# Performance work log

Hardware: AMD Instinct MI355X
Metric: run time of the kernel (lower is better)

Reference implementation:

```python
import jax, jax.numpy as jnp
import numpy as np

N, E, D, L, R = 100000, 500000, 128, 2, 10
EPS = 1e-5  # BatchNorm1d default eps


def setup_inputs() -> dict:
    key = jax.random.key(0)
    ks = jax.random.split(key, 10)
    return {
        "in_node_emb": jax.random.normal(ks[0], (N, D), jnp.float32),
        "in_rel_emb": jax.random.normal(ks[1], (R, D), jnp.float32),
        "w_in": jax.random.normal(ks[2], (L, D, D), jnp.float32) * 0.05,
        "w_out": jax.random.normal(ks[3], (L, D, D), jnp.float32) * 0.05,
        "w_loop": jax.random.normal(ks[4], (L, D, D), jnp.float32) * 0.05,
        "w_rel": jax.random.normal(ks[5], (L, D, D), jnp.float32) * 0.05,
        "loop_rel": jax.random.normal(ks[6], (L, 1, D), jnp.float32) * 0.05,
        "bias": jnp.zeros((L, D), jnp.float32),
        "edge_src": jax.random.randint(ks[7], (E,), 0, N),
        "edge_dst": jax.random.randint(ks[8], (E,), 0, N),
        "edge_type": jax.random.randint(ks[9], (E,), 0, R),
    }


def _gcn_forward(in_node_emb, in_rel_emb, w_in, w_out, w_loop, w_rel, loop_rel,
                 bias, edge_src, edge_dst, edge_type):
    x, r = in_node_emb, in_rel_emb
    ones_e = jnp.ones((E,), in_node_emb.dtype)
    for l in range(L):
        rel = jnp.concatenate([r, loop_rel[l]], axis=0)  # [R+1, D]; last row = self-loop relation
        rel_e = rel[edge_type]                            # [E, D] per-edge relation embedding

        def directed_msg(row, col, w):
            # gather -> compose ('mult') -> linear -> degree norm -> scatter-add at row
            comp = x[col] * rel_e                         # [E, D]
            m = comp @ w                                  # [E, D]
            deg = jnp.zeros((N,), x.dtype).at[row].add(ones_e)
            dinv = jnp.where(deg > 0, jax.lax.rsqrt(deg), 0.0)
            m = m * (dinv[row] * dinv[col])[:, None]
            return jnp.zeros((N, D), x.dtype).at[row].add(m)

        in_res = directed_msg(edge_src, edge_dst, w_in[l])   # original direction (src<-dst msgs)
        out_res = directed_msg(edge_dst, edge_src, w_out[l]) # mirrored direction
        loop_res = (x * loop_rel[l]) @ w_loop[l]             # self-loop (no norm)
        out = (in_res + out_res + loop_res) * (1.0 / 3.0) + bias[l]
        # BatchNorm1d over nodes, batch statistics, gamma=1 beta=0
        mean = out.mean(axis=0)
        var = out.var(axis=0)
        out = (out - mean) * jax.lax.rsqrt(var + EPS)
        x = jnp.tanh(out)
        r = (rel @ w_rel[l])[:-1]                            # transform rels, drop loop row
    return x, r


def reference(in_node_emb, in_rel_emb, w_in, w_out, w_loop, w_rel, loop_rel,
              bias, edge_src, edge_dst, edge_type):
    return _gcn_forward(in_node_emb, in_rel_emb, w_in, w_out, w_loop, w_rel,
                        loop_rel, bias, edge_src, edge_dst, edge_type)
```

## Files before the change

kernel.cpp:

```cpp
#include <hip/hip_runtime.h>
#include <math.h>

#define Nn 100000
#define Ee 500000
#define Dd 128
#define Rr 10
#define ND (Nn * Dd)
#define LDK 136
#define EPSF 1e-5f
#define XBLK (ND / 8 / 256)
#define EB ((Ee + 255) / 256)
#define SLOTS 32

typedef _Float16 half_t;
typedef __attribute__((ext_vector_type(2))) _Float16 h2;
typedef __attribute__((ext_vector_type(8))) _Float16 half8;
typedef __attribute__((ext_vector_type(4))) float f32x4;
typedef unsigned short ushort;
typedef unsigned int uint;
typedef unsigned long long u64;

union H8 { uint4 q; _Float16 h[8]; h2 p[4]; };

__device__ __forceinline__ void atomAddF(float* p, float v) {
    unsafeAtomicAdd(p, v);
}

__global__ void kzeroi(int* p, int n) {
    int i = blockIdx.x * blockDim.x + threadIdx.x;
    int stride = gridDim.x * blockDim.x;
    for (; i < n; i += stride) p[i] = 0;
}

__global__ __launch_bounds__(256) void kbin(
    const int* __restrict__ src, const int* __restrict__ dst,
    const int* __restrict__ typ,
    int* cnt_s, int* cnt_d, uint* __restrict__ rec_s, uint* __restrict__ rec_d,
    const float* __restrict__ x, const float* __restrict__ lr0,
    const float* __restrict__ w_in, const float* __restrict__ w_out,
    const float* __restrict__ w_loop, const float* __restrict__ w_rel,
    const float* __restrict__ r0,
    half_t* __restrict__ xb, half_t* __restrict__ xlb,
    half_t* __restrict__ Wt, half_t* __restrict__ rel0p, half_t* __restrict__ rel1p,
    float* __restrict__ r2out) {
    int blk = blockIdx.x;
    int tid = threadIdx.x;
    if (blk < EB) {
        int e = blk * 256 + tid;
        if (e >= Ee) return;
        int s = src[e], d = dst[e], t = typ[e];
        int ps = atomicAdd(&cnt_s[s], 1);
        if (ps < SLOTS) rec_s[((size_t)s << 5) | ps] = (uint)((d << 4) | t);
        int pd = atomicAdd(&cnt_d[d], 1);
        if (pd < SLOTS) rec_d[((size_t)d << 5) | pd] = (uint)((s << 4) | t);
    } else if (blk < EB + XBLK) {
        int idx = (blk - EB) * 256 + tid;
        int base = idx * 8;
        int k = base & 127;
        float4 v0 = *(const float4*)(x + base);
        float4 v1 = *(const float4*)(x + base + 4);
        float4 l0 = *(const float4*)(lr0 + k);
        float4 l1 = *(const float4*)(lr0 + k + 4);
        H8 xo, xl;
        xo.h[0] = (half_t)v0.x; xo.h[1] = (half_t)v0.y; xo.h[2] = (half_t)v0.z; xo.h[3] = (half_t)v0.w;
        xo.h[4] = (half_t)v1.x; xo.h[5] = (half_t)v1.y; xo.h[6] = (half_t)v1.z; xo.h[7] = (half_t)v1.w;
        xl.h[0] = (half_t)(v0.x * l0.x); xl.h[1] = (half_t)(v0.y * l0.y);
        xl.h[2] = (half_t)(v0.z * l0.z); xl.h[3] = (half_t)(v0.w * l0.w);
        xl.h[4] = (half_t)(v1.x * l1.x); xl.h[5] = (half_t)(v1.y * l1.y);
        xl.h[6] = (half_t)(v1.z * l1.z); xl.h[7] = (half_t)(v1.w * l1.w);
        *(uint4*)(xb + base) = xo.q;
        *(uint4*)(xlb + base) = xl.q;
    } else if (blk < EB + XBLK + 384) {
        int idx = (blk - EB - XBLK) * 256 + tid;
        int l = idx >= 49152;
        int rem = idx - l * 49152;
        int p = rem >> 14, ri = rem & 16383;
        int n = ri >> 7, k = ri & 127;
        const float* W = (p == 0) ? (w_in + l * 16384)
                       : ((p == 1) ? (w_out + l * 16384) : (w_loop + l * 16384));
        Wt[idx] = (half_t)W[k * 128 + n];
    } else if (blk == EB + XBLK + 384) {
        __shared__ float sr[Rr * Dd];
        for (int i = tid; i < Rr * Dd; i += 256) sr[i] = r0[i];
        __syncthreads();
        for (int ph = 0; ph < 2; ph++) {
            const float* w = w_rel + ph * 16384;
            float o[5];
#pragma unroll
            for (int q = 0; q < 5; q++) {
                int oi = tid + q * 256;
                int row = oi >> 7, j = oi & 127;
                float acc = 0.f;
                for (int k = 0; k < 128; k++) acc += sr[row * 128 + k] * w[k * 128 + j];
                o[q] = acc;
            }
            __syncthreads();
#pragma unroll
            for (int q = 0; q < 5; q++) {
                int oi = tid + q * 256;
                sr[oi] = o[q];
                if (ph == 0) rel1p[oi] = (half_t)o[q];
                else r2out[oi] = o[q];
            }
            __syncthreads();
        }
        for (int i = Rr * Dd + tid; i < 16 * Dd; i += 256) rel1p[i] = (half_t)0.f;
    } else {
        for (int i = tid; i < 16 * Dd; i += 256)
            rel0p[i] = (i < Rr * Dd) ? (half_t)r0[i] : (half_t)0.f;
    }
}

__global__ __launch_bounds__(256) void kgather(
    const int* __restrict__ cnt_s, const uint* __restrict__ rec_s,
    const int* __restrict__ cnt_d, const uint* __restrict__ rec_d,
    const half_t* __restrict__ xb, const half_t* __restrict__ relp,
    half_t* __restrict__ aggin, half_t* __restrict__ aggout, int gb) {
    __shared__ uint4 sRel[256];
    sRel[threadIdx.x] = ((const uint4*)relp)[threadIdx.x];
    __syncthreads();

    int blk = blockIdx.x;
    const int* cnt; const uint* rec; half_t* agg;
    if (blk < gb) { cnt = cnt_s; rec = rec_s; agg = aggin; }
    else { blk -= gb; cnt = cnt_d; rec = rec_d; agg = aggout; }
    int wv = threadIdx.x >> 6;
    int lane = threadIdx.x & 63;
    int nq = lane >> 4;
    int hl = lane & 15;
    int node = blk * 16 + wv * 4 + nq;
    bool valid = node < Nn;
    int nodec = valid ? node : (Nn - 1);
    int c = cnt[nodec];
    int n_it = valid ? min(c, SLOTS) : 0;
    const uint* rp = rec + ((size_t)nodec << 5);

    const uint4* x16 = (const uint4*)xb;
    float accf[8];
#pragma unroll
    for (int k = 0; k < 8; k++) accf[k] = 0.f;

    int it = 0;
    for (; it + 1 < n_it; it += 2) {
        uint r0 = rp[it];
        uint r1 = rp[it + 1];
        int nb0 = r0 >> 4, nb1 = r1 >> 4;
        int cn0 = cnt[nb0];
        int cn1 = cnt[nb1];
        H8 xv0, xv1, rv0, rv1;
        xv0.q = x16[(size_t)nb0 * 16 + hl];
        xv1.q = x16[(size_t)nb1 * 16 + hl];
        rv0.q = sRel[(r0 & 15u) * 16 + hl];
        rv1.q = sRel[(r1 & 15u) * 16 + hl];
        float w0 = (cn0 > 0) ? rsqrtf((float)cn0) : 0.f;
        float w1 = (cn1 > 0) ? rsqrtf((float)cn1) : 0.f;
#pragma unroll
        for (int k = 0; k < 8; k++)
            accf[k] += (float)xv0.h[k] * (float)rv0.h[k] * w0;
#pragma unroll
        for (int k = 0; k < 8; k++)
            accf[k] += (float)xv1.h[k] * (float)rv1.h[k] * w1;
    }
    if (it < n_it) {
        uint r0 = rp[it];
        int nb0 = r0 >> 4;
        int cn0 = cnt[nb0];
        H8 xv0, rv0;
        xv0.q = x16[(size_t)nb0 * 16 + hl];
        rv0.q = sRel[(r0 & 15u) * 16 + hl];
        float w0 = (cn0 > 0) ? rsqrtf((float)cn0) : 0.f;
#pragma unroll
        for (int k = 0; k < 8; k++)
            accf[k] += (float)xv0.h[k] * (float)rv0.h[k] * w0;
    }
    if (valid) {
        float wn = (c > 0) ? rsqrtf((float)c) : 0.f;
        H8 o;
#pragma unroll
        for (int k = 0; k < 8; k++) o.h[k] = (half_t)(accf[k] * wn);
        ((uint4*)agg)[(size_t)node * 16 + hl] = o.q;
    }
}

__global__ __launch_bounds__(256) void kmm(
    const half_t* __restrict__ aggin, const half_t* __restrict__ aggout,
    const half_t* __restrict__ xlb, const half_t* __restrict__ Wt,
    const float* __restrict__ bias, half_t* __restrict__ out,
    float* colsum, float* colsumsq) {
    __shared__ half_t sW[128 * LDK];
    const int tid = threadIdx.x;
    const int wv = tid >> 6;
    const int lane = tid & 63;
    const int col = lane & 15;
    const int quad = lane >> 4;
    const int m0 = blockIdx.x * 128;
    const int rowbase = m0 + wv * 32;

    f32x4 acc[2][8];
#pragma unroll
    for (int m = 0; m < 2; m++)
#pragma unroll
        for (int j = 0; j < 8; j++) acc[m][j] = (f32x4){0.f, 0.f, 0.f, 0.f};

    const half_t* Ap[3] = {aggin, aggout, xlb};
    int r0 = rowbase + col;
    int r1 = r0 + 16;
    int r0c = (r0 < Nn) ? r0 : (Nn - 1);
    int r1c = (r1 < Nn) ? r1 : (Nn - 1);

    for (int p = 0; p < 3; p++) {
        __syncthreads();
        {
            const half8* Wg = (const half8*)(Wt + p * 16384);
#pragma unroll
            for (int i = 0; i < 8; i++) {
                int c = tid + i * 256;
                int n = c >> 4, ko = (c & 15) * 8;
                *(half8*)(sW + n * LDK + ko) = Wg[c];
            }
        }
        __syncthreads();
        const half_t* A = Ap[p];
#pragma unroll
        for (int s = 0; s < 4; s++) {
            int ko = s * 32 + quad * 8;
            half8 va0 = *(const half8*)(A + r0c * Dd + ko);
            half8 va1 = *(const half8*)(A + r1c * Dd + ko);
#pragma unroll
            for (int j = 0; j < 8; j++) {
                half8 vb = *(const half8*)(sW + (j * 16 + col) * LDK + ko);
                acc[0][j] = __builtin_amdgcn_mfma_f32_16x16x32_f16(va0, vb, acc[0][j], 0, 0, 0);
                acc[1][j] = __builtin_amdgcn_mfma_f32_16x16x32_f16(va1, vb, acc[1][j], 0, 0, 0);
            }
        }
    }

    const float inv3 = 1.f / 3.f;
    float bcol[8], sum[8], ssq[8];
#pragma unroll
    for (int j = 0; j < 8; j++) {
        bcol[j] = bias[j * 16 + col];
        sum[j] = 0.f; ssq[j] = 0.f;
    }
#pragma unroll
    for (int m = 0; m < 2; m++) {
        int rb = rowbase + m * 16;
        if (rb < Nn) {
#pragma unroll
            for (int j = 0; j < 8; j++) {
#pragma unroll
                for (int r = 0; r < 4; r++) {
                    float v = acc[m][j][r] * inv3 + bcol[j];
                    out[(rb + quad * 4 + r) * Dd + j * 16 + col] = (half_t)v;
                    sum[j] += v;
                    ssq[j] += v * v;
                }
            }
        }
    }
#pragma unroll
    for (int j = 0; j < 8; j++) {
        sum[j] += __shfl_xor(sum[j], 16, 64);
        sum[j] += __shfl_xor(sum[j], 32, 64);
        ssq[j] += __shfl_xor(ssq[j], 16, 64);
        ssq[j] += __shfl_xor(ssq[j], 32, 64);
    }
    __syncthreads();
    float* sred = (float*)sW;
    if (quad == 0) {
#pragma unroll
        for (int j = 0; j < 8; j++) {
            sred[wv * 128 + j * 16 + col] = sum[j];
            sred[512 + wv * 128 + j * 16 + col] = ssq[j];
        }
    }
    __syncthreads();
    if (tid < 128) {
        float s = 0.f, s2 = 0.f;
#pragma unroll
        for (int w = 0; w < 4; w++) {
            s += sred[w * 128 + tid];
            s2 += sred[512 + w * 128 + tid];
        }
        atomAddF(&colsum[tid], s);
        atomAddF(&colsumsq[tid], s2);
    }
}

__global__ __launch_bounds__(256) void knorm0(const half_t* __restrict__ outh,
                                              const float* __restrict__ colsum,
                                              const float* __restrict__ colsumsq,
                                              const float* __restrict__ lr,
                                              half_t* __restrict__ xb,
                                              half_t* __restrict__ xlb) {
    __shared__ float sm[128], srs[128];
    int tid = threadIdx.x;
    if (tid < 128) {
        float m = colsum[tid] * (1.f / (float)Nn);
        float v = colsumsq[tid] * (1.f / (float)Nn) - m * m;
        sm[tid] = m;
        srs[tid] = rsqrtf(v + EPSF);
    }
    __syncthreads();
    int idx = blockIdx.x * 256 + tid;
    int base = idx * 8;
    int k = base & 127;
    H8 v; v.q = *(const uint4*)(outh + base);
    H8 xo, xl;
#pragma unroll
    for (int q = 0; q < 8; q++) {
        float t = tanhf(((float)v.h[q] - sm[k + q]) * srs[k + q]);
        xo.h[q] = (half_t)t;
        xl.h[q] = (half_t)(t * lr[k + q]);
    }
    *(uint4*)(xb + base) = xo.q;
    *(uint4*)(xlb + base) = xl.q;
}

__global__ __launch_bounds__(256) void knorm1(const half_t* __restrict__ outh,
                                              const float* __restrict__ colsum,
                                              const float* __restrict__ colsumsq,
                                              float* __restrict__ xn) {
    __shared__ float sm[128], srs[128];
    int tid = threadIdx.x;
    if (tid < 128) {
        float m = colsum[tid] * (1.f / (float)Nn);
        float v = colsumsq[tid] * (1.f / (float)Nn) - m * m;
        sm[tid] = m;
        srs[tid] = rsqrtf(v + EPSF);
    }
    __syncthreads();
    int idx = blockIdx.x * 256 + tid;
    int base = idx * 8;
    int k = base & 127;
    H8 v; v.q = *(const uint4*)(outh + base);
    float4 o0, o1;
    o0.x = tanhf(((float)v.h[0] - sm[k + 0]) * srs[k + 0]);
    o0.y = tanhf(((float)v.h[1] - sm[k + 1]) * srs[k + 1]);
    o0.z = tanhf(((float)v.h[2] - sm[k + 2]) * srs[k + 2]);
    o0.w = tanhf(((float)v.h[3] - sm[k + 3]) * srs[k + 3]);
    o1.x = tanhf(((float)v.h[4] - sm[k + 4]) * srs[k + 4]);
    o1.y = tanhf(((float)v.h[5] - sm[k + 5]) * srs[k + 5]);
    o1.z = tanhf(((float)v.h[6] - sm[k + 6]) * srs[k + 6]);
    o1.w = tanhf(((float)v.h[7] - sm[k + 7]) * srs[k + 7]);
    *(float4*)(xn + base) = o0;
    *(float4*)(xn + base + 4) = o1;
}

extern "C" void kernel_launch(void* const* d_in, const int* in_sizes, int n_in,
                              void* d_out, int out_size, void* d_ws, size_t ws_size,
                              hipStream_t stream) {
    const float* x0      = (const float*)d_in[0];
    const float* r0      = (const float*)d_in[1];
    const float* w_in    = (const float*)d_in[2];
    const float* w_out   = (const float*)d_in[3];
    const float* w_loop  = (const float*)d_in[4];
    const float* w_rel   = (const float*)d_in[5];
    const float* looprel = (const float*)d_in[6];
    const float* bias    = (const float*)d_in[7];
    const int* esrc = (const int*)d_in[8];
    const int* edst = (const int*)d_in[9];
    const int* etyp = (const int*)d_in[10];
    float* outp = (float*)d_out;

    half_t* us = (half_t*)d_ws;
    half_t* aggin_h  = us;
    half_t* aggout_h = us + (size_t)ND;
    half_t* xb       = us + 2 * (size_t)ND;
    half_t* xlb      = us + 3 * (size_t)ND;
    half_t* outh     = us + 4 * (size_t)ND;
    half_t* Wt       = us + 5 * (size_t)ND;
    half_t* rel0p    = Wt + 2 * 49152;
    half_t* rel1p    = rel0p + 16 * Dd;
    uint* rec_s = (uint*)(rel1p + 16 * Dd);
    uint* rec_d = rec_s + (size_t)Nn * SLOTS;
    int* cnt_s  = (int*)(rec_d + (size_t)Nn * SLOTS);
    int* cnt_d  = cnt_s + Nn;
    float* colsumA = (float*)(cnt_d + Nn);
    float* colsumB = colsumA + 2 * Dd;

    kzeroi<<<256, 256, 0, stream>>>(cnt_s, 2 * Nn + 4 * Dd);
    kbin<<<EB + XBLK + 386, 256, 0, stream>>>(
        esrc, edst, etyp, cnt_s, cnt_d, rec_s, rec_d,
        x0, looprel, w_in, w_out, w_loop, w_rel, r0,
        xb, xlb, Wt, rel0p, rel1p, outp + (size_t)ND);

    const int gb = (Nn + 15) / 16;
    for (int l = 0; l < 2; l++) {
        const half_t* relp = l ? rel1p : rel0p;
        float* cs = l ? colsumB : colsumA;
        kgather<<<2 * gb, 256, 0, stream>>>(cnt_s, rec_s, cnt_d, rec_d,
                                            xb, relp, aggin_h, aggout_h, gb);
        kmm<<<(Nn + 127) / 128, 256, 0, stream>>>(aggin_h, aggout_h, xlb, Wt + l * 49152,
                                                  bias + l * Dd, outh, cs, cs + Dd);
        if (l == 0) {
            knorm0<<<ND / 8 / 256, 256, 0, stream>>>(outh, cs, cs + Dd, looprel + Dd, xb, xlb);
        } else {
            knorm1<<<ND / 8 / 256, 256, 0, stream>>>(outh, cs, cs + Dd, outp);
        }
    }
}
```

Measured before the change: 440.5 us.

## Assign one wavefront per node in gather and split edges across lane groups

The gather kernel now maps one 64-lane wavefront to each node instead of four nodes per wavefront. The four 16-lane groups take interleaved slices of the node's edge list and are combined with cross-lane shuffles. This balances work across degree variation and cuts the serial per-node loop length, in exchange for four times as many blocks and idle groups on low-degree nodes. The bin kernel also moves the serial relation-transform block to the front of the grid so it starts early rather than being a late straggler.

```diff
diff --git a/kernel.cpp b/kernel.cpp
--- a/kernel.cpp
+++ b/kernel.cpp
@@ -45,16 +45,55 @@
     float* __restrict__ r2out) {
     int blk = blockIdx.x;
     int tid = threadIdx.x;
-    if (blk < EB) {
-        int e = blk * 256 + tid;
+    if (blk == 0) {
+        __shared__ float sr[Rr * Dd];
+        for (int i = tid; i < Rr * Dd; i += 256) sr[i] = r0[i];
+        __syncthreads();
+        for (int ph = 0; ph < 2; ph++) {
+            const float* w = w_rel + ph * 16384;
+            float o[5];
+#pragma unroll
+            for (int q = 0; q < 5; q++) {
+                int oi = tid + q * 256;
+                int row = oi >> 7, j = oi & 127;
+                float acc = 0.f;
+#pragma unroll 4
+                for (int k = 0; k < 128; k++) acc += sr[row * 128 + k] * w[k * 128 + j];
+                o[q] = acc;
+            }
+            __syncthreads();
+#pragma unroll
+            for (int q = 0; q < 5; q++) {
+                int oi = tid + q * 256;
+                sr[oi] = o[q];
+                if (ph == 0) rel1p[oi] = (half_t)o[q];
+                else r2out[oi] = o[q];
+            }
+            __syncthreads();
+        }
+        for (int i = Rr * Dd + tid; i < 16 * Dd; i += 256) rel1p[i] = (half_t)0.f;
+    } else if (blk == 1) {
+        for (int i = tid; i < 16 * Dd; i += 256)
+            rel0p[i] = (i < Rr * Dd) ? (half_t)r0[i] : (half_t)0.f;
+    } else if (blk < 386) {
+        int idx = (blk - 2) * 256 + tid;
+        int l = idx >= 49152;
+        int rem = idx - l * 49152;
+        int p = rem >> 14, ri = rem & 16383;
+        int n = ri >> 7, k = ri & 127;
+        const float* W = (p == 0) ? (w_in + l * 16384)
+                       : ((p == 1) ? (w_out + l * 16384) : (w_loop + l * 16384));
+        Wt[idx] = (half_t)W[k * 128 + n];
+    } else if (blk < 386 + EB) {
+        int e = (blk - 386) * 256 + tid;
         if (e >= Ee) return;
         int s = src[e], d = dst[e], t = typ[e];
         int ps = atomicAdd(&cnt_s[s], 1);
         if (ps < SLOTS) rec_s[((size_t)s << 5) | ps] = (uint)((d << 4) | t);
         int pd = atomicAdd(&cnt_d[d], 1);
         if (pd < SLOTS) rec_d[((size_t)d << 5) | pd] = (uint)((s << 4) | t);
-    } else if (blk < EB + XBLK) {
-        int idx = (blk - EB) * 256 + tid;
+    } else {
+        int idx = (blk - 386 - EB) * 256 + tid;
         int base = idx * 8;
         int k = base & 127;
         float4 v0 = *(const float4*)(x + base);
@@ -70,44 +109,6 @@
         xl.h[6] = (half_t)(v1.z * l1.z); xl.h[7] = (half_t)(v1.w * l1.w);
         *(uint4*)(xb + base) = xo.q;
         *(uint4*)(xlb + base) = xl.q;
-    } else if (blk < EB + XBLK + 384) {
-        int idx = (blk - EB - XBLK) * 256 + tid;
-        int l = idx >= 49152;
-        int rem = idx - l * 49152;
-        int p = rem >> 14, ri = rem & 16383;
-        int n = ri >> 7, k = ri & 127;
-        const float* W = (p == 0) ? (w_in + l * 16384)
-                       : ((p == 1) ? (w_out + l * 16384) : (w_loop + l * 16384));
-        Wt[idx] = (half_t)W[k * 128 + n];
-    } else if (blk == EB + XBLK + 384) {
-        __shared__ float sr[Rr * Dd];
-        for (int i = tid; i < Rr * Dd; i += 256) sr[i] = r0[i];
-        __syncthreads();
-        for (int ph = 0; ph < 2; ph++) {
-            const float* w = w_rel + ph * 16384;
-            float o[5];
-#pragma unroll
-            for (int q = 0; q < 5; q++) {
-                int oi = tid + q * 256;
-                int row = oi >> 7, j = oi & 127;
-                float acc = 0.f;
-                for (int k = 0; k < 128; k++) acc += sr[row * 128 + k] * w[k * 128 + j];
-                o[q] = acc;
-            }
-            __syncthreads();
-#pragma unroll
-            for (int q = 0; q < 5; q++) {
-                int oi = tid + q * 256;
-                sr[oi] = o[q];
-                if (ph == 0) rel1p[oi] = (half_t)o[q];
-                else r2out[oi] = o[q];
-            }
-            __syncthreads();
-        }
-        for (int i = Rr * Dd + tid; i < 16 * Dd; i += 256) rel1p[i] = (half_t)0.f;
-    } else {
-        for (int i = tid; i < 16 * Dd; i += 256)
-            rel0p[i] = (i < Rr * Dd) ? (half_t)r0[i] : (half_t)0.f;
     }
 }
 
@@ -126,24 +127,22 @@
     else { blk -= gb; cnt = cnt_d; rec = rec_d; agg = aggout; }
     int wv = threadIdx.x >> 6;
     int lane = threadIdx.x & 63;
-    int nq = lane >> 4;
+    int grp = lane >> 4;
     int hl = lane & 15;
-    int node = blk * 16 + wv * 4 + nq;
-    bool valid = node < Nn;
-    int nodec = valid ? node : (Nn - 1);
-    int c = cnt[nodec];
-    int n_it = valid ? min(c, SLOTS) : 0;
-    const uint* rp = rec + ((size_t)nodec << 5);
+    int node = blk * 4 + wv;
+    int c = cnt[node];
+    int n = min(c, SLOTS);
+    const uint* rp = rec + ((size_t)node << 5);
 
     const uint4* x16 = (const uint4*)xb;
     float accf[8];
 #pragma unroll
     for (int k = 0; k < 8; k++) accf[k] = 0.f;
 
-    int it = 0;
-    for (; it + 1 < n_it; it += 2) {
+    int it = grp;
+    for (; it + 4 < n; it += 8) {
         uint r0 = rp[it];
-        uint r1 = rp[it + 1];
+        uint r1 = rp[it + 4];
         int nb0 = r0 >> 4, nb1 = r1 >> 4;
         int cn0 = cnt[nb0];
         int cn1 = cnt[nb1];
@@ -161,7 +160,7 @@
         for (int k = 0; k < 8; k++)
             accf[k] += (float)xv1.h[k] * (float)rv1.h[k] * w1;
     }
-    if (it < n_it) {
+    if (it < n) {
         uint r0 = rp[it];
         int nb0 = r0 >> 4;
         int cn0 = cnt[nb0];
@@ -173,7 +172,12 @@
         for (int k = 0; k < 8; k++)
             accf[k] += (float)xv0.h[k] * (float)rv0.h[k] * w0;
     }
-    if (valid) {
+#pragma unroll
+    for (int k = 0; k < 8; k++) {
+        accf[k] += __shfl_xor(accf[k], 16, 64);
+        accf[k] += __shfl_xor(accf[k], 32, 64);
+    }
+    if (lane < 16) {
         float wn = (c > 0) ? rsqrtf((float)c) : 0.f;
         H8 o;
 #pragma unroll
@@ -380,12 +384,12 @@
     float* colsumB = colsumA + 2 * Dd;
 
     kzeroi<<<256, 256, 0, stream>>>(cnt_s, 2 * Nn + 4 * Dd);
-    kbin<<<EB + XBLK + 386, 256, 0, stream>>>(
+    kbin<<<386 + EB + XBLK, 256, 0, stream>>>(
         esrc, edst, etyp, cnt_s, cnt_d, rec_s, rec_d,
         x0, looprel, w_in, w_out, w_loop, w_rel, r0,
         xb, xlb, Wt, rel0p, rel1p, outp + (size_t)ND);
 
-    const int gb = (Nn + 15) / 16;
+    const int gb = Nn / 4;
     for (int l = 0; l < 2; l++) {
         const half_t* relp = l ? rel1p : rel0p;
         float* cs = l ? colsumB : colsumA;
```

Result: slower. 517.5 us (+17.5%).
